# Performance work log

Measured on AMD Instinct MI355X. Metric: run time of the kernel, lower is better.

## Reference

```python
import jax, jax.numpy as jnp
import numpy as np

B, S, V, D, E, F, H, HS, TOPK = 8, 512, 32000, 1024, 8, 4096, 8, 128, 2
NEG = -1e9


def _ln(x, g, b):
    m = x.mean(-1, keepdims=True)
    v = jnp.var(x, axis=-1, keepdims=True)
    return (x - m) * jax.lax.rsqrt(v + 1e-5) * g + b


def _attn(x, Wq, Wk, Wv, Wo, bo):
    q = (x @ Wq).reshape(B, S, H, HS)
    k = (x @ Wk).reshape(B, S, H, HS)
    v = (x @ Wv).reshape(B, S, H, HS)
    att = jnp.einsum('bqhd,bkhd->bhqk', q, k) * (HS ** -0.5)
    causal = jnp.tril(jnp.ones((S, S), bool))
    att = jax.nn.softmax(jnp.where(causal, att, NEG), axis=-1)
    o = jnp.einsum('bhqk,bkhd->bqhd', att, v).reshape(B, S, H * HS)
    return o @ Wo + bo


def _moe(x, noise, Wr, br, Wn, bn, W1, b1, W2, b2):
    # NoisyTopkRouter: logits + randn * softplus(noise_logits), top-k, -inf fill, softmax
    logits = x @ Wr + br                                   # [B,S,E]
    noisy = logits + noise * jax.nn.softplus(x @ Wn + bn)
    _, idx = jax.lax.top_k(noisy, TOPK)                    # [B,S,K]
    mask = jax.nn.one_hot(idx, E, dtype=jnp.bool_).any(-2)  # [B,S,E]
    gate = jax.nn.softmax(jnp.where(mask, noisy, NEG), axis=-1)
    # dense all-expert FFN; combine with gate (gate==0 for non-selected experts,
    # so this equals the original sparse per-expert dispatch/scatter math)
    xf = x.reshape(-1, D)                                   # [T,D]
    gf = gate.reshape(-1, E)                                # [T,E]
    h = jax.nn.relu(jnp.einsum('td,edf->etf', xf, W1) + b1[:, None, :])
    y = jnp.einsum('etf,efd->etd', h, W2) + b2[:, None, :]
    out = jnp.einsum('etd,te->td', y, gf).reshape(x.shape)
    return out, gate


def setup_inputs() -> dict:
    key = jax.random.key(0)
    ks = jax.random.split(key, 24)
    n = lambda i, shp, sc=0.02: jax.random.normal(ks[i], shp, jnp.float32) * sc
    return dict(
        input_ids=jax.random.randint(ks[0], (B, S), 0, V),
        attention_mask=jnp.ones((B, S), jnp.int32),
        emb=n(1, (V, D), 1.0),
        pos=n(2, (1, S, D), 1.0),
        Wq=n(3, (D, H * HS)), Wk=n(4, (D, H * HS)), Wv=n(5, (D, H * HS)),
        Wo=n(6, (H * HS, D)), bo=jnp.zeros((D,)),
        g1=jnp.ones((D,)), be1=jnp.zeros((D,)),
        g2=jnp.ones((D,)), be2=jnp.zeros((D,)),
        g3=jnp.ones((D,)), be3=jnp.zeros((D,)),
        Wr1=n(7, (D, E)), br1=jnp.zeros((E,)), Wn1=n(8, (D, E)), bn1=jnp.zeros((E,)),
        W1a=n(9, (E, D, F)), b1a=jnp.zeros((E, F)), W2a=n(10, (E, F, D)), b2a=jnp.zeros((E, D)),
        Wr2=n(11, (D, E)), br2=jnp.zeros((E,)), Wn2=n(12, (D, E)), bn2=jnp.zeros((E,)),
        W1b=n(13, (E, D, F)), b1b=jnp.zeros((E, F)), W2b=n(14, (E, F, D)), b2b=jnp.zeros((E, D)),
        noise1=jax.random.normal(ks[15], (B, S, E), jnp.float32),
        noise2=jax.random.normal(ks[16], (B, S, E), jnp.float32),
        Wc=n(17, (D, 10)), bc=jnp.zeros((10,)),
    )


def reference(input_ids, attention_mask, emb, pos, Wq, Wk, Wv, Wo, bo,
              g1, be1, g2, be2, g3, be3,
              Wr1, br1, Wn1, bn1, W1a, b1a, W2a, b2a,
              Wr2, br2, Wn2, bn2, W1b, b1b, W2b, b2b,
              noise1, noise2, Wc, bc):
    x = emb[input_ids]                                     # [B,S,D]
    x = x + _attn(_ln(x, g1, be1), Wq, Wk, Wv, Wo, bo)
    x = x + pos                                            # dropout = identity (eval)
    first, _ = _moe(_ln(x, g2, be2), noise1, Wr1, br1, Wn1, bn1, W1a, b1a, W2a, b2a)
    second, _ = _moe(_ln(x, g3, be3), noise2, Wr2, br2, Wn2, bn2, W1b, b1b, W2b, b2b)
    feature = second.mean(axis=1)                          # [B,D]
    cls = feature @ Wc + bc                                # [B,10]
    return (first, second, feature, cls)
```

## Files before the change

### kernel.cpp

```cpp
#include <hip/hip_runtime.h>
#include <cstdint>

typedef unsigned short u16;
typedef __attribute__((ext_vector_type(8))) __bf16 bf16x8;
typedef __attribute__((ext_vector_type(4))) float f32x4;

#define TOK 4096
#define DM  1024
#define EXP 8
#define FF  4096
#define SEQ 512
#define NH  8
#define HD  128
#define JOBCAP 18432

__device__ __forceinline__ u16 f2bf(float f) {
  union { float f; unsigned int u; } v; v.f = f;
  unsigned int u = v.u;
  u += 0x7FFFu + ((u >> 16) & 1u);
  return (u16)(u >> 16);
}
__device__ __forceinline__ float bf2f(u16 h) {
  union { unsigned int u; float f; } v; v.u = ((unsigned int)h) << 16; return v.f;
}

__device__ __forceinline__ void gl_lds16(const u16* g, u16* l) {
  __builtin_amdgcn_global_load_lds(
      (const __attribute__((address_space(1))) unsigned int*)g,
      (__attribute__((address_space(3))) unsigned int*)l, 16, 0, 0);
}

__global__ void k_embed(const int* __restrict__ ids, const float* __restrict__ emb,
                        float* __restrict__ x) {
  int t = blockIdx.x;
  int id = ids[t];
  const float4* src = (const float4*)(emb + (size_t)id * DM);
  float4* dst = (float4*)(x + (size_t)t * DM);
  dst[threadIdx.x] = src[threadIdx.x];
}

__global__ void k_lnrouter(const float* __restrict__ xin, const float* __restrict__ g,
                           const float* __restrict__ be,
                           const float* __restrict__ Wr, const float* __restrict__ br,
                           const float* __restrict__ Wn, const float* __restrict__ bn,
                           const float* __restrict__ noise,
                           u16* __restrict__ obf,
                           float* __restrict__ gates, int* __restrict__ topidx) {
  int t = blockIdx.x, tid = threadIdx.x;
  float4 v = ((const float4*)(xin + (size_t)t * DM))[tid];
  float s = v.x + v.y + v.z + v.w;
  float sq = v.x*v.x + v.y*v.y + v.z*v.z + v.w*v.w;
  for (int o = 32; o; o >>= 1) { s += __shfl_down(s, o); sq += __shfl_down(sq, o); }
  __shared__ float ss[4], sqs[4];
  if ((tid & 63) == 0) { ss[tid >> 6] = s; sqs[tid >> 6] = sq; }
  __syncthreads();
  s  = ss[0] + ss[1] + ss[2] + ss[3];
  sq = sqs[0] + sqs[1] + sqs[2] + sqs[3];
  float mean = s * (1.f / DM);
  float var  = sq * (1.f / DM) - mean * mean;
  float rstd = rsqrtf(var + 1e-5f);
  float4 gg = ((const float4*)g)[tid];
  float4 bb = ((const float4*)be)[tid];
  float xl[4];
  xl[0] = (v.x - mean) * rstd * gg.x + bb.x;
  xl[1] = (v.y - mean) * rstd * gg.y + bb.y;
  xl[2] = (v.z - mean) * rstd * gg.z + bb.z;
  xl[3] = (v.w - mean) * rstd * gg.w + bb.w;
  ushort4 u;
  u.x = f2bf(xl[0]); u.y = f2bf(xl[1]); u.z = f2bf(xl[2]); u.w = f2bf(xl[3]);
  ((ushort4*)(obf + (size_t)t * DM))[tid] = u;

  float pl[8], pn[8];
  #pragma unroll
  for (int e = 0; e < 8; e++) { pl[e] = 0.f; pn[e] = 0.f; }
  #pragma unroll
  for (int j = 0; j < 4; j++) {
    int d = tid * 4 + j;
    float xv = xl[j];
    const float4* wr = (const float4*)(Wr + (size_t)d * 8);
    const float4* wn = (const float4*)(Wn + (size_t)d * 8);
    float4 a0 = wr[0], a1 = wr[1], c0 = wn[0], c1 = wn[1];
    pl[0] += xv * a0.x; pl[1] += xv * a0.y; pl[2] += xv * a0.z; pl[3] += xv * a0.w;
    pl[4] += xv * a1.x; pl[5] += xv * a1.y; pl[6] += xv * a1.z; pl[7] += xv * a1.w;
    pn[0] += xv * c0.x; pn[1] += xv * c0.y; pn[2] += xv * c0.z; pn[3] += xv * c0.w;
    pn[4] += xv * c1.x; pn[5] += xv * c1.y; pn[6] += xv * c1.z; pn[7] += xv * c1.w;
  }
  for (int o = 32; o; o >>= 1) {
    #pragma unroll
    for (int e = 0; e < 8; e++) { pl[e] += __shfl_down(pl[e], o); pn[e] += __shfl_down(pn[e], o); }
  }
  __shared__ float sl[4][8], sn[4][8];
  if ((tid & 63) == 0) {
    int w = tid >> 6;
    #pragma unroll
    for (int e = 0; e < 8; e++) { sl[w][e] = pl[e]; sn[w][e] = pn[e]; }
  }
  __syncthreads();
  if (tid == 0) {
    float noisy[8];
    #pragma unroll
    for (int e = 0; e < 8; e++) {
      float l  = sl[0][e] + sl[1][e] + sl[2][e] + sl[3][e] + br[e];
      float nn = sn[0][e] + sn[1][e] + sn[2][e] + sn[3][e] + bn[e];
      float sp = (nn > 20.f) ? nn : log1pf(expf(nn));
      noisy[e] = l + noise[(size_t)t * 8 + e] * sp;
    }
    int i0 = 0;
    for (int e = 1; e < 8; e++) if (noisy[e] > noisy[i0]) i0 = e;
    int i1 = (i0 == 0) ? 1 : 0;
    for (int e = 0; e < 8; e++) if (e != i0 && noisy[e] > noisy[i1]) i1 = e;
    float e1 = expf(noisy[i1] - noisy[i0]);
    float zz = 1.f + e1;
    gates[t * 2] = 1.f / zz; gates[t * 2 + 1] = e1 / zz;
    topidx[t * 2] = i0; topidx[t * 2 + 1] = i1;
  }
}

__global__ void k_ln2(const float* __restrict__ in, const float* __restrict__ g,
                      const float* __restrict__ be, u16* __restrict__ oh,
                      u16* __restrict__ ol) {
  int t = blockIdx.x, tid = threadIdx.x;
  float4 v = ((const float4*)(in + (size_t)t * DM))[tid];
  float s = v.x + v.y + v.z + v.w;
  float sq = v.x*v.x + v.y*v.y + v.z*v.z + v.w*v.w;
  for (int o = 32; o; o >>= 1) { s += __shfl_down(s, o); sq += __shfl_down(sq, o); }
  __shared__ float ss[4], sqs[4];
  if ((tid & 63) == 0) { ss[tid >> 6] = s; sqs[tid >> 6] = sq; }
  __syncthreads();
  s  = ss[0] + ss[1] + ss[2] + ss[3];
  sq = sqs[0] + sqs[1] + sqs[2] + sqs[3];
  float mean = s * (1.f / DM);
  float var  = sq * (1.f / DM) - mean * mean;
  float rstd = rsqrtf(var + 1e-5f);
  float4 gg = ((const float4*)g)[tid];
  float4 bb = ((const float4*)be)[tid];
  float o4[4];
  o4[0] = (v.x - mean) * rstd * gg.x + bb.x;
  o4[1] = (v.y - mean) * rstd * gg.y + bb.y;
  o4[2] = (v.z - mean) * rstd * gg.z + bb.z;
  o4[3] = (v.w - mean) * rstd * gg.w + bb.w;
  ushort4 uh, ul;
  u16* ph = (u16*)&uh; u16* pl = (u16*)&ul;
  #pragma unroll
  for (int i = 0; i < 4; i++) {
    u16 hi = f2bf(o4[i]); ph[i] = hi; pl[i] = f2bf(o4[i] - bf2f(hi));
  }
  ((ushort4*)(oh + (size_t)t * DM))[tid] = uh;
  ((ushort4*)(ol + (size_t)t * DM))[tid] = ul;
}

__global__ void k_tcvt_split(const float* __restrict__ src, u16* __restrict__ dh,
                             u16* __restrict__ dl, int K, int N) {
  __shared__ float t[32][33];
  int k0 = blockIdx.x * 32, n0 = blockIdx.y * 32;
  int tx = threadIdx.x, ty = threadIdx.y;
  #pragma unroll
  for (int i = 0; i < 4; i++) t[ty + 8*i][tx] = src[(size_t)(k0 + ty + 8*i) * N + n0 + tx];
  __syncthreads();
  int u = ty * 32 + tx;
  int r = u >> 3, kq = u & 7;
  ushort4 oh, ol;
  u16* ph = (u16*)&oh; u16* pl = (u16*)&ol;
  #pragma unroll
  for (int i = 0; i < 4; i++) {
    float v = t[kq*4+i][r];
    u16 hi = f2bf(v); ph[i] = hi; pl[i] = f2bf(v - bf2f(hi));
  }
  *(ushort4*)&dh[(size_t)(n0 + r) * K + k0 + kq*4] = oh;
  *(ushort4*)&dl[(size_t)(n0 + r) * K + k0 + kq*4] = ol;
}

__global__ void k_tcvt64(const float* __restrict__ srcA, const float* __restrict__ srcB,
                         u16* __restrict__ dst, int K, int N) {
  __shared__ float t[64][65];
  int z = blockIdx.z;
  const float* src = (z < 8) ? srcA + (size_t)z * K * N : srcB + (size_t)(z - 8) * K * N;
  u16* d = dst + (size_t)z * K * N;
  int k0 = blockIdx.x * 64, n0 = blockIdx.y * 64;
  int u = threadIdx.y * 32 + threadIdx.x;
  #pragma unroll
  for (int i = 0; i < 4; i++) {
    int idx = u + i * 256;
    int kr = idx >> 4, nq = (idx & 15) * 4;
    float4 v = *(const float4*)&src[(size_t)(k0 + kr) * N + n0 + nq];
    t[kr][nq] = v.x; t[kr][nq+1] = v.y; t[kr][nq+2] = v.z; t[kr][nq+3] = v.w;
  }
  __syncthreads();
  #pragma unroll
  for (int j = 0; j < 2; j++) {
    int idx = u + j * 256;
    int nr = idx >> 3, kq = (idx & 7) * 8;
    ushort4 o0, o1;
    u16* p0 = (u16*)&o0; u16* p1 = (u16*)&o1;
    #pragma unroll
    for (int i = 0; i < 4; i++) p0[i] = f2bf(t[kq + i][nr]);
    #pragma unroll
    for (int i = 0; i < 4; i++) p1[i] = f2bf(t[kq + 4 + i][nr]);
    *(ushort4*)&d[(size_t)(n0 + nr) * K + k0 + kq]     = o0;
    *(ushort4*)&d[(size_t)(n0 + nr) * K + k0 + kq + 4] = o1;
  }
}

__global__ void k_softmax_h(float* __restrict__ scores) {
  int q = blockIdx.x, bh = blockIdx.y, tid = threadIdx.x;
  float* row = scores + ((size_t)bh * 512 + q) * 512;
  u16* orow = (u16*)row;
  const float scale = 0.088388347648318447f;
  int j0 = tid * 2;
  float v0 = -1e30f, v1 = -1e30f;
  if (j0 <= q)     v0 = row[j0] * scale;
  if (j0 + 1 <= q) v1 = row[j0 + 1] * scale;
  float m = fmaxf(v0, v1);
  for (int o = 32; o; o >>= 1) m = fmaxf(m, __shfl_down(m, o));
  __shared__ float sm[4], ssum[4];
  if ((tid & 63) == 0) sm[tid >> 6] = m;
  __syncthreads();
  m = fmaxf(fmaxf(sm[0], sm[1]), fmaxf(sm[2], sm[3]));
  float p0 = (j0 <= q)     ? expf(v0 - m) : 0.f;
  float p1 = (j0 + 1 <= q) ? expf(v1 - m) : 0.f;
  float s = p0 + p1;
  for (int o = 32; o; o >>= 1) s += __shfl_down(s, o);
  if ((tid & 63) == 0) ssum[tid >> 6] = s;
  __syncthreads();
  s = ssum[0] + ssum[1] + ssum[2] + ssum[3];
  float inv = 1.f / s;
  float pi0 = p0 * inv, pi1 = p1 * inv;
  u16 h0 = f2bf(pi0), h1 = f2bf(pi1);
  orow[j0]       = h0; orow[j0 + 1]       = h1;
  orow[512 + j0] = f2bf(pi0 - bf2f(h0));
  orow[512 + j0 + 1] = f2bf(pi1 - bf2f(h1));
}

constexpr int HOP_QKV    = 0;
constexpr int HOP_SCORES = 1;
constexpr int HOP_PV     = 2;
constexpr int HOP_PROJ   = 3;

struct GemmHArgs {
  const u16 *Ah, *Al, *Bh, *Bl;
  u16 *D0h, *D0l, *D1h, *D1l, *D2h, *D2l;
  float *Cf;
  const float *bias, *resid, *pos;
  int lda, ldb, K;
};

template<int OP>
__launch_bounds__(256)
__global__ void gemm_h(GemmHArgs p) {
  int bx, by, z;
  if constexpr (OP == HOP_QKV) {
    int bid = blockIdx.x; int xcd = bid & 7, slot = bid >> 3;
    by = xcd * 3 + (slot >> 5); bx = slot & 31; z = 0;
  } else if constexpr (OP == HOP_PROJ) {
    int bid = blockIdx.x; by = bid & 7; bx = bid >> 3; z = 0;
  } else if constexpr (OP == HOP_SCORES) {
    int bid = blockIdx.x; z = bid / 10; int t = bid % 10;
    bx = (t >= 6) ? 3 : (t >= 3) ? 2 : (t >= 1) ? 1 : 0;
    by = t - ((bx * (bx + 1)) >> 1);
  } else {
    bx = blockIdx.x; by = blockIdx.y; z = blockIdx.z;
  }

  const u16 *Ahb, *Alb, *Bhb, *Blb;
  if constexpr (OP == HOP_SCORES) {
    size_t off = (size_t)(z >> 3) * 524288 + (size_t)(z & 7) * 128;
    Ahb = p.Ah + off; Alb = p.Al + off; Bhb = p.Bh + off; Blb = p.Bl + off;
  } else if constexpr (OP == HOP_PV) {
    size_t aoff = (size_t)z * 524288;
    Ahb = p.Ah + aoff; Alb = p.Ah + aoff + 512;
    size_t boff = (size_t)z * 65536;
    Bhb = p.Bh + boff; Blb = p.Bl + boff;
  } else {
    Ahb = p.Ah; Alb = p.Al; Bhb = p.Bh; Blb = p.Bl;
  }

  int kmax = p.K;
  if constexpr (OP == HOP_PV) { int lim = bx * 128 + 128; kmax = lim < p.K ? lim : p.K; }
  int nt = kmax >> 5;

  __shared__ __align__(16) u16 As[2 * 4096];
  __shared__ __align__(16) u16 Bs[2 * 4096];

  int tid = threadIdx.x, lane = tid & 63, wid = tid >> 6;
  int srow = wid * 16 + (lane >> 2), skoff = (lane & 3) * 8;
  int lo0 = (wid * 16) * 32, lo1 = ((wid + 4) * 16) * 32;
  int wr = wid >> 1, wc = wid & 1, fm = lane & 15, fk = (lane >> 4) * 8;

  f32x4 acc[4][4] = {};
  const size_t lda = p.lda, ldb = p.ldb;

  #pragma unroll 1
  for (int pass = 0; pass < 3; ++pass) {
    const u16* Ab = (pass < 2) ? Ahb : Alb;
    const u16* Bb = (pass & 1) ? Blb : Bhb;
    const u16* aptr0 = Ab + (size_t)(bx * 128 + srow) * lda + skoff;
    const u16* aptr1 = Ab + (size_t)(bx * 128 + 64 + srow) * lda + skoff;
    const u16* bptr0 = Bb + (size_t)(by * 128 + srow) * ldb + skoff;
    const u16* bptr1 = Bb + (size_t)(by * 128 + 64 + srow) * ldb + skoff;

    gl_lds16(aptr0, &As[lo0]); gl_lds16(aptr1, &As[lo1]);
    gl_lds16(bptr0, &Bs[lo0]); gl_lds16(bptr1, &Bs[lo1]);
    __syncthreads();
    int cur = 0;
    for (int t = 0; t < nt; ++t) {
      if (t + 1 < nt) {
        int nxt = (cur ^ 1) * 4096;
        int k0 = (t + 1) * 32;
        gl_lds16(aptr0 + k0, &As[nxt + lo0]); gl_lds16(aptr1 + k0, &As[nxt + lo1]);
        gl_lds16(bptr0 + k0, &Bs[nxt + lo0]); gl_lds16(bptr1 + k0, &Bs[nxt + lo1]);
      }
      int cb = cur * 4096;
      bf16x8 af[4], bfr[4];
      #pragma unroll
      for (int i = 0; i < 4; ++i) {
        af[i]  = *(const bf16x8*)&As[cb + (wr * 64 + i * 16 + fm) * 32 + fk];
        bfr[i] = *(const bf16x8*)&Bs[cb + (wc * 64 + i * 16 + fm) * 32 + fk];
      }
      #pragma unroll
      for (int mi = 0; mi < 4; ++mi)
        #pragma unroll
        for (int ni = 0; ni < 4; ++ni)
          acc[mi][ni] = __builtin_amdgcn_mfma_f32_16x16x32_bf16(af[mi], bfr[ni], acc[mi][ni], 0, 0, 0);
      __syncthreads();
      cur ^= 1;
    }
  }

  int rb = (lane >> 4) * 4, cl = lane & 15;
  #pragma unroll
  for (int mi = 0; mi < 4; ++mi)
    #pragma unroll
    for (int ni = 0; ni < 4; ++ni)
      #pragma unroll
      for (int j = 0; j < 4; ++j) {
        int m = bx * 128 + wr * 64 + mi * 16 + rb + j;
        int n = by * 128 + wc * 64 + ni * 16 + cl;
        float v = acc[mi][ni][j];
        if constexpr (OP == HOP_QKV) {
          u16 hi = f2bf(v); u16 lo = f2bf(v - bf2f(hi));
          int sel = n >> 10, nn = n & 1023;
          if (sel == 0) {
            p.D0h[(size_t)m * DM + nn] = hi; p.D0l[(size_t)m * DM + nn] = lo;
          } else if (sel == 1) {
            p.D1h[(size_t)m * DM + nn] = hi; p.D1l[(size_t)m * DM + nn] = lo;
          } else {
            size_t idx = (size_t)((m >> 9) * 8 + (nn >> 7)) * 65536 + (size_t)(nn & 127) * 512 + (m & 511);
            p.D2h[idx] = hi; p.D2l[idx] = lo;
          }
        } else if constexpr (OP == HOP_SCORES) {
          p.Cf[(size_t)z * 262144 + (size_t)m * 512 + n] = v;
        } else if constexpr (OP == HOP_PV) {
          u16 hi = f2bf(v); u16 lo = f2bf(v - bf2f(hi));
          size_t idx = (size_t)(z >> 3) * 524288 + (size_t)m * 1024 + (size_t)(z & 7) * 128 + n;
          p.D0h[idx] = hi; p.D0l[idx] = lo;
        } else {
          size_t idx = (size_t)m * 1024 + n;
          p.Cf[idx] = v + p.bias[n] + p.resid[idx] + p.pos[(size_t)(m & 511) * 1024 + n];
        }
      }
}

constexpr int OP_MOE1 = 0;
constexpr int OP_MOE2 = 1;

struct GemmArgs {
  const u16* A; const u16* B; void* C;
  const float* b1a; const float* b1b;
  const int* joblist; const int* seg;
  int lda, ldb, K;
};

template<int OP>
__launch_bounds__(256)
__global__ void gemm_k(GemmArgs p) {
  int bid = blockIdx.x;
  int xcd = bid & 7, slot = bid >> 3;
  int bx, by;
  if constexpr (OP == OP_MOE1) {
    by = xcd * 4 + (slot & 3);
    bx = slot >> 2;
  } else {
    bx = xcd * 18 + (slot >> 3);
    by = slot & 7;
  }
  int r0g = bx * 128;
  if (r0g >= p.seg[16]) return;
  int z = 0;
  #pragma unroll
  for (int e = 1; e < 16; ++e) z += (r0g >= p.seg[e]) ? 1 : 0;
  const u16* Bbase = p.B + (size_t)z * 4194304;
  const float* bias = (z < 8) ? p.b1a + (size_t)z * (OP == OP_MOE1 ? FF : DM)
                              : p.b1b + (size_t)(z - 8) * (OP == OP_MOE1 ? FF : DM);

  __shared__ __align__(16) u16 As[2 * 4096];
  __shared__ __align__(16) u16 Bs[2 * 4096];

  int tid = threadIdx.x;
  int lane = tid & 63, wid = tid >> 6;

  int srow = wid * 16 + (lane >> 2);
  int skoff = (lane & 3) * 8;

  const u16 *aptr0, *aptr1;
  if constexpr (OP == OP_MOE1) {
    int j0 = p.joblist[r0g + srow];
    int j1 = p.joblist[r0g + 64 + srow];
    aptr0 = p.A + (size_t)(j0 < 0 ? 0 : j0) * p.lda + skoff;
    aptr1 = p.A + (size_t)(j1 < 0 ? 0 : j1) * p.lda + skoff;
  } else {
    aptr0 = p.A + (size_t)(r0g + srow) * p.lda + skoff;
    aptr1 = p.A + (size_t)(r0g + 64 + srow) * p.lda + skoff;
  }
  const u16* bptr0 = Bbase + (size_t)(by * 128 + srow) * p.ldb + skoff;
  const u16* bptr1 = Bbase + (size_t)(by * 128 + 64 + srow) * p.ldb + skoff;

  int lo0 = (wid * 16) * 32;
  int lo1 = ((wid + 4) * 16) * 32;

  int wr = wid >> 1, wc = wid & 1;
  int fm = lane & 15;
  int fk = (lane >> 4) * 8;

  f32x4 acc[4][4] = {};
  int nt = p.K >> 5;

  gl_lds16(aptr0, &As[lo0]); gl_lds16(aptr1, &As[lo1]);
  gl_lds16(bptr0, &Bs[lo0]); gl_lds16(bptr1, &Bs[lo1]);
  __syncthreads();

  int cur = 0;
  for (int t = 0; t < nt; ++t) {
    if (t + 1 < nt) {
      int nxt = (cur ^ 1) * 4096;
      int k0 = (t + 1) * 32;
      gl_lds16(aptr0 + k0, &As[nxt + lo0]); gl_lds16(aptr1 + k0, &As[nxt + lo1]);
      gl_lds16(bptr0 + k0, &Bs[nxt + lo0]); gl_lds16(bptr1 + k0, &Bs[nxt + lo1]);
    }
    int cb = cur * 4096;
    bf16x8 af[4], bfr[4];
    #pragma unroll
    for (int i = 0; i < 4; ++i) {
      af[i]  = *(const bf16x8*)&As[cb + (wr * 64 + i * 16 + fm) * 32 + fk];
      bfr[i] = *(const bf16x8*)&Bs[cb + (wc * 64 + i * 16 + fm) * 32 + fk];
    }
    #pragma unroll
    for (int mi = 0; mi < 4; ++mi)
      #pragma unroll
      for (int ni = 0; ni < 4; ++ni)
        acc[mi][ni] = __builtin_amdgcn_mfma_f32_16x16x32_bf16(af[mi], bfr[ni], acc[mi][ni], 0, 0, 0);
    __syncthreads();
    cur ^= 1;
  }

  int rb = (lane >> 4) * 4;
  int cl = lane & 15;
  #pragma unroll
  for (int mi = 0; mi < 4; ++mi)
    #pragma unroll
    for (int ni = 0; ni < 4; ++ni)
      #pragma unroll
      for (int j = 0; j < 4; ++j) {
        int m = r0g + wr * 64 + mi * 16 + rb + j;
        int n = by * 128 + wc * 64 + ni * 16 + cl;
        float v = acc[mi][ni][j];
        if constexpr (OP == OP_MOE1) {
          float t2 = v + bias[n];
          t2 = t2 > 0.f ? t2 : 0.f;
          ((u16*)p.C)[(size_t)m * FF + n] = f2bf(t2);
        } else {
          ((float*)p.C)[(size_t)m * DM + n] = v + bias[n];
        }
      }
}

__global__ void k_moe_init(int* cnt, int* cnt2, int* joblist) {
  int i = blockIdx.x * 256 + threadIdx.x;
  if (i < JOBCAP) joblist[i] = -1;
  if (i < 16) { cnt[i] = 0; cnt2[i] = 0; }
}
__global__ void k_moe_count(const int* __restrict__ topidx, int* __restrict__ cnt) {
  int t = blockIdx.x * 256 + threadIdx.x;
  if (t >= 2 * TOK) return;
  int lo = (t >= TOK) ? 8 : 0;
  atomicAdd(&cnt[topidx[t * 2] + lo], 1);
  atomicAdd(&cnt[topidx[t * 2 + 1] + lo], 1);
}
__global__ void k_moe_offsets(const int* __restrict__ cnt, int* __restrict__ seg) {
  if (threadIdx.x == 0) {
    int o = 0;
    for (int e = 0; e < 16; e++) { seg[e] = o; o += (cnt[e] + 127) & ~127; }
    seg[16] = o;
  }
}
__global__ void k_moe_scatter(const int* __restrict__ topidx, int* __restrict__ cnt2,
                              const int* __restrict__ seg, int* __restrict__ joblist,
                              int* __restrict__ tokpos) {
  int t = blockIdx.x * 256 + threadIdx.x;
  if (t >= 2 * TOK) return;
  int lo = (t >= TOK) ? 8 : 0;
  #pragma unroll
  for (int s = 0; s < 2; s++) {
    int e = topidx[t * 2 + s] + lo;
    int p = atomicAdd(&cnt2[e], 1);
    int pos = seg[e] + p;
    joblist[pos] = t;
    tokpos[t * 2 + s] = pos;
  }
}
__global__ void k_combine(const float* __restrict__ y, const float* __restrict__ gates,
                          const int* __restrict__ tokpos, float* __restrict__ out) {
  int t = blockIdx.x, tid = threadIdx.x;
  int p0 = tokpos[t * 2], p1 = tokpos[t * 2 + 1];
  float g0 = gates[t * 2], g1 = gates[t * 2 + 1];
  float4 a = ((const float4*)(y + (size_t)p0 * DM))[tid];
  float4 b = ((const float4*)(y + (size_t)p1 * DM))[tid];
  float4 o;
  o.x = g0 * a.x + g1 * b.x; o.y = g0 * a.y + g1 * b.y;
  o.z = g0 * a.z + g1 * b.z; o.w = g0 * a.w + g1 * b.w;
  ((float4*)(out + (size_t)t * DM))[tid] = o;
}

__global__ void k_feat1(const float* __restrict__ second, float* __restrict__ part) {
  int b = blockIdx.x, c = blockIdx.y, tid = threadIdx.x;
  const float* p = second + ((size_t)b * SEQ + (size_t)c * 64) * DM;
  float4 s = {0.f, 0.f, 0.f, 0.f};
  for (int j = 0; j < 64; ++j) {
    float4 v = ((const float4*)(p + (size_t)j * DM))[tid];
    s.x += v.x; s.y += v.y; s.z += v.z; s.w += v.w;
  }
  ((float4*)(part + (size_t)(b * 8 + c) * DM))[tid] = s;
}
__global__ void k_feat2(const float* __restrict__ part, float* __restrict__ feat) {
  int i = blockIdx.x * 256 + threadIdx.x;
  int b = i >> 10, d = i & 1023;
  float s = 0.f;
  #pragma unroll
  for (int c = 0; c < 8; ++c) s += part[(size_t)(b * 8 + c) * DM + d];
  feat[i] = s * (1.f / SEQ);
}
__global__ void k_cls(const float* __restrict__ feat, const float* __restrict__ Wc,
                      const float* __restrict__ bc, float* __restrict__ cls) {
  int o = blockIdx.x; int b = o / 10, n = o % 10; int l = threadIdx.x;
  float s = 0.f;
  for (int d = l; d < DM; d += 64) s += feat[b * DM + d] * Wc[(size_t)d * 10 + n];
  for (int off = 32; off; off >>= 1) s += __shfl_down(s, off);
  if (l == 0) cls[o] = s + bc[n];
}

extern "C" void kernel_launch(void* const* d_in, const int* in_sizes, int n_in,
                              void* d_out, int out_size, void* d_ws, size_t ws_size,
                              hipStream_t stream) {
  const int*   ids    = (const int*)d_in[0];
  const float* emb    = (const float*)d_in[2];
  const float* pos    = (const float*)d_in[3];
  const float* Wq     = (const float*)d_in[4];
  const float* Wk     = (const float*)d_in[5];
  const float* Wv     = (const float*)d_in[6];
  const float* Wo     = (const float*)d_in[7];
  const float* bo     = (const float*)d_in[8];
  const float* g1     = (const float*)d_in[9];
  const float* be1    = (const float*)d_in[10];
  const float* g2     = (const float*)d_in[11];
  const float* be2    = (const float*)d_in[12];
  const float* g3     = (const float*)d_in[13];
  const float* be3    = (const float*)d_in[14];
  const float* Wr1    = (const float*)d_in[15];
  const float* br1    = (const float*)d_in[16];
  const float* Wn1    = (const float*)d_in[17];
  const float* bn1    = (const float*)d_in[18];
  const float* W1a    = (const float*)d_in[19];
  const float* b1a    = (const float*)d_in[20];
  const float* W2a    = (const float*)d_in[21];
  const float* b2a    = (const float*)d_in[22];
  const float* Wr2    = (const float*)d_in[23];
  const float* br2    = (const float*)d_in[24];
  const float* Wn2    = (const float*)d_in[25];
  const float* bn2    = (const float*)d_in[26];
  const float* W1b    = (const float*)d_in[27];
  const float* b1b    = (const float*)d_in[28];
  const float* W2b    = (const float*)d_in[29];
  const float* b2b    = (const float*)d_in[30];
  const float* noise1 = (const float*)d_in[31];
  const float* noise2 = (const float*)d_in[32];
  const float* Wc     = (const float*)d_in[33];
  const float* bc     = (const float*)d_in[34];

  char* wsp = (char*)d_ws; size_t off = 0;
  auto alloc = [&](size_t bytes) -> void* {
    void* p = wsp + off; off += (bytes + 255) & ~(size_t)255; return p;
  };
  char*  G     = (char*)alloc(360710144);
  float* x     = (float*)alloc((size_t)TOK * DM * 4);
  float* x2    = (float*)alloc((size_t)TOK * DM * 4);
  u16*   xlnb  = (u16*)alloc((size_t)2 * TOK * DM * 2);
  float* gates  = (float*)alloc(2 * TOK * 2 * 4);
  int*   topidx = (int*)alloc(2 * TOK * 2 * 4);
  int*   cnt    = (int*)alloc(16 * 4);
  int*   cnt2   = (int*)alloc(16 * 4);
  int*   seg    = (int*)alloc(24 * 4);
  int*   joblist= (int*)alloc(JOBCAP * 4);
  int*   tokpos = (int*)alloc(2 * TOK * 2 * 4);
  float* fpart  = (float*)alloc(64 * DM * 4);
  (void)ws_size; (void)in_sizes; (void)n_in; (void)out_size;

  u16* WQKVTh = (u16*)(G + 0);
  u16* WQKVTl = (u16*)(G + 6291456);
  u16* WOTh   = (u16*)(G + 12582912);
  u16* WOTl   = (u16*)(G + 14680064);
  u16* XLNH   = (u16*)(G + 16777216);
  u16* XLNL   = (u16*)(G + 25165824);
  u16* QH     = (u16*)(G + 33554432);
  u16* QL     = (u16*)(G + 41943040);
  u16* KH     = (u16*)(G + 50331648);
  u16* KL     = (u16*)(G + 58720256);
  u16* VTh    = (u16*)(G + 67108864);
  u16* VTl    = (u16*)(G + 75497472);
  u16* OH     = (u16*)(G + 83886080);
  u16* OL     = (u16*)(G + 92274688);
  float* SC   = (float*)(G + 100663296);
  u16*   H    = (u16*)(G + 0);
  float* Y    = (float*)(G + 150994944);
  u16*   WBUF = (u16*)(G + 226492416);

  float* out_first  = (float*)d_out;
  float* out_second = out_first + (size_t)TOK * DM;
  float* feat       = out_first + (size_t)2 * TOK * DM;
  float* cls        = feat + 8 * DM;

  dim3 tb(32, 8);
  hipLaunchKernelGGL(k_tcvt_split, dim3(32, 32), tb, 0, stream, Wq, WQKVTh,            WQKVTl,            DM, DM);
  hipLaunchKernelGGL(k_tcvt_split, dim3(32, 32), tb, 0, stream, Wk, WQKVTh + 1048576,  WQKVTl + 1048576,  DM, DM);
  hipLaunchKernelGGL(k_tcvt_split, dim3(32, 32), tb, 0, stream, Wv, WQKVTh + 2097152,  WQKVTl + 2097152,  DM, DM);
  hipLaunchKernelGGL(k_tcvt_split, dim3(32, 32), tb, 0, stream, Wo, WOTh,              WOTl,              DM, DM);
  hipLaunchKernelGGL(k_embed, dim3(TOK), dim3(256), 0, stream, ids, emb, x);
  hipLaunchKernelGGL(k_ln2, dim3(TOK), dim3(256), 0, stream, x, g1, be1, XLNH, XLNL);

  GemmHArgs qa{};
  qa.Ah = XLNH; qa.Al = XLNL; qa.Bh = WQKVTh; qa.Bl = WQKVTl;
  qa.D0h = QH; qa.D0l = QL; qa.D1h = KH; qa.D1l = KL; qa.D2h = VTh; qa.D2l = VTl;
  qa.lda = DM; qa.ldb = DM; qa.K = DM;
  hipLaunchKernelGGL(gemm_h<HOP_QKV>, dim3(768), dim3(256), 0, stream, qa);

  GemmHArgs sa{};
  sa.Ah = QH; sa.Al = QL; sa.Bh = KH; sa.Bl = KL; sa.Cf = SC;
  sa.lda = DM; sa.ldb = DM; sa.K = HD;
  hipLaunchKernelGGL(gemm_h<HOP_SCORES>, dim3(640), dim3(256), 0, stream, sa);
  hipLaunchKernelGGL(k_softmax_h, dim3(SEQ, 64), dim3(256), 0, stream, SC);

  GemmHArgs pa{};
  pa.Ah = (const u16*)SC; pa.Bh = VTh; pa.Bl = VTl;
  pa.D0h = OH; pa.D0l = OL;
  pa.lda = 1024; pa.ldb = 512; pa.K = SEQ;
  hipLaunchKernelGGL(gemm_h<HOP_PV>, dim3(4, 1, 64), dim3(256), 0, stream, pa);

  GemmHArgs pj{};
  pj.Ah = OH; pj.Al = OL; pj.Bh = WOTh; pj.Bl = WOTl; pj.Cf = x2;
  pj.bias = bo; pj.resid = x; pj.pos = pos;
  pj.lda = DM; pj.ldb = DM; pj.K = DM;
  hipLaunchKernelGGL(gemm_h<HOP_PROJ>, dim3(256), dim3(256), 0, stream, pj);

  hipLaunchKernelGGL(k_lnrouter, dim3(TOK), dim3(256), 0, stream, x2, g2, be2,
                     Wr1, br1, Wn1, bn1, noise1, xlnb, gates, topidx);
  hipLaunchKernelGGL(k_lnrouter, dim3(TOK), dim3(256), 0, stream, x2, g3, be3,
                     Wr2, br2, Wn2, bn2, noise2, xlnb + (size_t)TOK * DM,
                     gates + (size_t)TOK * 2, topidx + (size_t)TOK * 2);
  hipLaunchKernelGGL(k_moe_init, dim3(72), dim3(256), 0, stream, cnt, cnt2, joblist);
  hipLaunchKernelGGL(k_moe_count, dim3(32), dim3(256), 0, stream, topidx, cnt);
  hipLaunchKernelGGL(k_moe_offsets, dim3(1), dim3(64), 0, stream, cnt, seg);
  hipLaunchKernelGGL(k_moe_scatter, dim3(32), dim3(256), 0, stream, topidx, cnt2, seg, joblist, tokpos);

  hipLaunchKernelGGL(k_tcvt64, dim3(16, 64, 16), tb, 0, stream, W1a, W1b, WBUF, DM, FF);
  GemmArgs m1{};
  m1.A = xlnb; m1.B = WBUF; m1.C = H; m1.b1a = b1a; m1.b1b = b1b;
  m1.joblist = joblist; m1.seg = seg;
  m1.lda = DM; m1.ldb = DM; m1.K = DM;
  hipLaunchKernelGGL(gemm_k<OP_MOE1>, dim3(4608), dim3(256), 0, stream, m1);

  hipLaunchKernelGGL(k_tcvt64, dim3(64, 16, 16), tb, 0, stream, W2a, W2b, WBUF, FF, DM);
  GemmArgs m2{};
  m2.A = H; m2.B = WBUF; m2.C = Y; m2.b1a = b2a; m2.b1b = b2b;
  m2.joblist = joblist; m2.seg = seg;
  m2.lda = FF; m2.ldb = FF; m2.K = FF;
  hipLaunchKernelGGL(gemm_k<OP_MOE2>, dim3(1152), dim3(256), 0, stream, m2);

  hipLaunchKernelGGL(k_combine, dim3(TOK), dim3(256), 0, stream, Y, gates, tokpos, out_first);
  hipLaunchKernelGGL(k_combine, dim3(TOK), dim3(256), 0, stream, Y,
                     gates + (size_t)TOK * 2, tokpos + (size_t)TOK * 2, out_second);

  hipLaunchKernelGGL(k_feat1, dim3(8, 8), dim3(256), 0, stream, out_second, fpart);
  hipLaunchKernelGGL(k_feat2, dim3(32), dim3(256), 0, stream, fpart, feat);
  hipLaunchKernelGGL(k_cls, dim3(80), dim3(64), 0, stream, feat, Wc, bc, cls);
}
```

Baseline: 1.179 ms.

## Deepen MoE GEMM k-tile to 64 with XOR-swizzled LDS and merge weight converts

The MoE grouped GEMM now stages 64-wide K tiles instead of 32. Each wave loads 4 row chunks per operand, and the LDS layout is XOR-swizzled to avoid bank conflicts on fragment reads. This halves the number of barrier iterations and makes each load batch larger, at the cost of doubling LDS use per block (64 KB), which may reduce occupancy. Separately, the four attention weight transpose-split launches are merged into a single launch using a z-grid dimension, cutting launch overhead.

```diff
diff --git a/kernel.cpp b/kernel.cpp
--- a/kernel.cpp
+++ b/kernel.cpp
@@ -149,25 +149,31 @@
   ((ushort4*)(ol + (size_t)t * DM))[tid] = ul;
 }
 
-__global__ void k_tcvt_split(const float* __restrict__ src, u16* __restrict__ dh,
-                             u16* __restrict__ dl, int K, int N) {
+__global__ void k_tcvt_split4(const float* __restrict__ Wq, const float* __restrict__ Wk,
+                              const float* __restrict__ Wv, const float* __restrict__ Wo,
+                              u16* __restrict__ qkvh, u16* __restrict__ qkvl,
+                              u16* __restrict__ oh, u16* __restrict__ ol) {
   __shared__ float t[32][33];
+  int z = blockIdx.z;
+  const float* src = (z == 0) ? Wq : (z == 1) ? Wk : (z == 2) ? Wv : Wo;
+  u16* dh = (z < 3) ? qkvh + (size_t)z * DM * DM : oh;
+  u16* dl = (z < 3) ? qkvl + (size_t)z * DM * DM : ol;
   int k0 = blockIdx.x * 32, n0 = blockIdx.y * 32;
   int tx = threadIdx.x, ty = threadIdx.y;
   #pragma unroll
-  for (int i = 0; i < 4; i++) t[ty + 8*i][tx] = src[(size_t)(k0 + ty + 8*i) * N + n0 + tx];
+  for (int i = 0; i < 4; i++) t[ty + 8*i][tx] = src[(size_t)(k0 + ty + 8*i) * DM + n0 + tx];
   __syncthreads();
   int u = ty * 32 + tx;
   int r = u >> 3, kq = u & 7;
-  ushort4 oh, ol;
-  u16* ph = (u16*)&oh; u16* pl = (u16*)&ol;
+  ushort4 ohv, olv;
+  u16* ph = (u16*)&ohv; u16* pl = (u16*)&olv;
   #pragma unroll
   for (int i = 0; i < 4; i++) {
     float v = t[kq*4+i][r];
     u16 hi = f2bf(v); ph[i] = hi; pl[i] = f2bf(v - bf2f(hi));
   }
-  *(ushort4*)&dh[(size_t)(n0 + r) * K + k0 + kq*4] = oh;
-  *(ushort4*)&dl[(size_t)(n0 + r) * K + k0 + kq*4] = ol;
+  *(ushort4*)&dh[(size_t)(n0 + r) * DM + k0 + kq*4] = ohv;
+  *(ushort4*)&dl[(size_t)(n0 + r) * DM + k0 + kq*4] = olv;
 }
 
 __global__ void k_tcvt64(const float* __restrict__ srcA, const float* __restrict__ srcB,
@@ -392,65 +398,70 @@
   const float* bias = (z < 8) ? p.b1a + (size_t)z * (OP == OP_MOE1 ? FF : DM)
                               : p.b1b + (size_t)(z - 8) * (OP == OP_MOE1 ? FF : DM);
 
-  __shared__ __align__(16) u16 As[2 * 4096];
-  __shared__ __align__(16) u16 Bs[2 * 4096];
+  __shared__ __align__(16) u16 As[2 * 8192];
+  __shared__ __align__(16) u16 Bs[2 * 8192];
 
   int tid = threadIdx.x;
   int lane = tid & 63, wid = tid >> 6;
 
-  int srow = wid * 16 + (lane >> 2);
-  int skoff = (lane & 3) * 8;
-
-  const u16 *aptr0, *aptr1;
-  if constexpr (OP == OP_MOE1) {
-    int j0 = p.joblist[r0g + srow];
-    int j1 = p.joblist[r0g + 64 + srow];
-    aptr0 = p.A + (size_t)(j0 < 0 ? 0 : j0) * p.lda + skoff;
-    aptr1 = p.A + (size_t)(j1 < 0 ? 0 : j1) * p.lda + skoff;
-  } else {
-    aptr0 = p.A + (size_t)(r0g + srow) * p.lda + skoff;
-    aptr1 = p.A + (size_t)(r0g + 64 + srow) * p.lda + skoff;
-  }
-  const u16* bptr0 = Bbase + (size_t)(by * 128 + srow) * p.ldb + skoff;
-  const u16* bptr1 = Bbase + (size_t)(by * 128 + 64 + srow) * p.ldb + skoff;
-
-  int lo0 = (wid * 16) * 32;
-  int lo1 = ((wid + 4) * 16) * 32;
+  int lr = lane >> 3;
+  int skq = (((lane & 7) ^ lr) * 8);
+
+  const u16 *aptr[4], *bptr[4];
+  #pragma unroll
+  for (int c = 0; c < 4; ++c) {
+    int row = wid * 32 + c * 8 + lr;
+    if constexpr (OP == OP_MOE1) {
+      int j = p.joblist[r0g + row];
+      aptr[c] = p.A + (size_t)(j < 0 ? 0 : j) * p.lda + skq;
+    } else {
+      aptr[c] = p.A + (size_t)(r0g + row) * p.lda + skq;
+    }
+    bptr[c] = Bbase + (size_t)(by * 128 + row) * p.ldb + skq;
+  }
+  int lbase = wid * 2048;
 
   int wr = wid >> 1, wc = wid & 1;
   int fm = lane & 15;
-  int fk = (lane >> 4) * 8;
+  int hi = lane >> 4;
+  int f7 = fm & 7;
 
   f32x4 acc[4][4] = {};
-  int nt = p.K >> 5;
-
-  gl_lds16(aptr0, &As[lo0]); gl_lds16(aptr1, &As[lo1]);
-  gl_lds16(bptr0, &Bs[lo0]); gl_lds16(bptr1, &Bs[lo1]);
+  int nt = p.K >> 6;
+
+#define STAGE(BUF, K0) {                                                     \
+    u16* a_ = &As[(BUF) * 8192 + lbase]; u16* b_ = &Bs[(BUF) * 8192 + lbase];\
+    _Pragma("unroll") for (int c = 0; c < 4; ++c) {                          \
+      gl_lds16(aptr[c] + (K0), a_ + c * 512);                                \
+      gl_lds16(bptr[c] + (K0), b_ + c * 512);                                \
+    } }
+
+  STAGE(0, 0);
   __syncthreads();
 
   int cur = 0;
   for (int t = 0; t < nt; ++t) {
-    if (t + 1 < nt) {
-      int nxt = (cur ^ 1) * 4096;
-      int k0 = (t + 1) * 32;
-      gl_lds16(aptr0 + k0, &As[nxt + lo0]); gl_lds16(aptr1 + k0, &As[nxt + lo1]);
-      gl_lds16(bptr0 + k0, &Bs[nxt + lo0]); gl_lds16(bptr1 + k0, &Bs[nxt + lo1]);
+    if (t + 1 < nt) STAGE(cur ^ 1, (t + 1) * 64);
+    int cb = cur * 8192;
+    #pragma unroll
+    for (int ks = 0; ks < 2; ++ks) {
+      int q = ((ks * 4 + hi) ^ f7) * 8;
+      bf16x8 af[4], bfr[4];
+      #pragma unroll
+      for (int i = 0; i < 4; ++i) {
+        af[i]  = *(const bf16x8*)&As[cb + (wr * 64 + i * 16 + fm) * 64 + q];
+        bfr[i] = *(const bf16x8*)&Bs[cb + (wc * 64 + i * 16 + fm) * 64 + q];
+      }
+      #pragma unroll
+      for (int mi = 0; mi < 4; ++mi)
+        #pragma unroll
+        for (int ni = 0; ni < 4; ++ni)
+          acc[mi][ni] = __builtin_amdgcn_mfma_f32_16x16x32_bf16(af[mi], bfr[ni], acc[mi][ni], 0, 0, 0);
     }
-    int cb = cur * 4096;
-    bf16x8 af[4], bfr[4];
-    #pragma unroll
-    for (int i = 0; i < 4; ++i) {
-      af[i]  = *(const bf16x8*)&As[cb + (wr * 64 + i * 16 + fm) * 32 + fk];
-      bfr[i] = *(const bf16x8*)&Bs[cb + (wc * 64 + i * 16 + fm) * 32 + fk];
-    }
-    #pragma unroll
-    for (int mi = 0; mi < 4; ++mi)
-      #pragma unroll
-      for (int ni = 0; ni < 4; ++ni)
-        acc[mi][ni] = __builtin_amdgcn_mfma_f32_16x16x32_bf16(af[mi], bfr[ni], acc[mi][ni], 0, 0, 0);
     __syncthreads();
     cur ^= 1;
   }
+#undef STAGE
 
   int rb = (lane >> 4) * 4;
   int cl = lane & 15;
@@ -628,10 +639,8 @@
   float* cls        = feat + 8 * DM;
 
   dim3 tb(32, 8);
-  hipLaunchKernelGGL(k_tcvt_split, dim3(32, 32), tb, 0, stream, Wq, WQKVTh,            WQKVTl,            DM, DM);
-  hipLaunchKernelGGL(k_tcvt_split, dim3(32, 32), tb, 0, stream, Wk, WQKVTh + 1048576,  WQKVTl + 1048576,  DM, DM);
-  hipLaunchKernelGGL(k_tcvt_split, dim3(32, 32), tb, 0, stream, Wv, WQKVTh + 2097152,  WQKVTl + 2097152,  DM, DM);
-  hipLaunchKernelGGL(k_tcvt_split, dim3(32, 32), tb, 0, stream, Wo, WOTh,              WOTl,              DM, DM);
+  hipLaunchKernelGGL(k_tcvt_split4, dim3(32, 32, 4), tb, 0, stream, Wq, Wk, Wv, Wo,
+                     WQKVTh, WQKVTl, WOTh, WOTl);
   hipLaunchKernelGGL(k_embed, dim3(TOK), dim3(256), 0, stream, ids, emb, x);
   hipLaunchKernelGGL(k_ln2, dim3(TOK), dim3(256), 0, stream, x, g1, be1, XLNH, XLNL);
 
```

Measured after the change: 1.216 ms. 3.2% more time.
